# Optimization experiments

Hardware: AMD Instinct MI355X
Metric: run time of the kernel (lower is better)

Reference implementation:

```python
import jax, jax.numpy as jnp
import numpy as np

N_NODES = 50000
N_EDGES = 800000
HIDDEN = 128
IN_DIM = 128
OUT_DIM = 40
N_LAYERS = 3


def setup_inputs() -> dict:
    key = jax.random.key(0)
    ks = jax.random.split(key, 8)
    s = 1.0 / np.sqrt(HIDDEN)
    return {
        "x": jax.random.normal(ks[0], (N_NODES, IN_DIM), jnp.float32),
        "edge_index": jax.random.randint(ks[1], (2, N_EDGES), 0, N_NODES, jnp.int32),
        "W_in": jax.random.normal(ks[2], (IN_DIM, HIDDEN), jnp.float32) * s,
        "b_in": jnp.zeros((HIDDEN,), jnp.float32),
        "Wl": jax.random.normal(ks[3], (N_LAYERS, HIDDEN, HIDDEN), jnp.float32) * s,
        "Wr": jax.random.normal(ks[4], (N_LAYERS, HIDDEN, HIDDEN), jnp.float32) * s,
        "bl": jnp.zeros((N_LAYERS, HIDDEN), jnp.float32),
        "Wc1": jax.random.normal(ks[5], (HIDDEN, HIDDEN), jnp.float32) * s,
        "bc1": jnp.zeros((HIDDEN,), jnp.float32),
        "Wc2": jax.random.normal(ks[6], (HIDDEN, OUT_DIM), jnp.float32) * s,
        "bc2": jnp.zeros((OUT_DIM,), jnp.float32),
    }


def reference(x, edge_index, W_in, b_in, Wl, Wr, bl, Wc1, bc1, Wc2, bc2):
    src, dst = edge_index[0], edge_index[1]
    n = x.shape[0]
    # in-degree for mean aggregation (clamped to 1 for isolated nodes)
    deg = jax.ops.segment_sum(jnp.ones_like(src, x.dtype), dst, num_segments=n)
    deg_inv = (1.0 / jnp.maximum(deg, 1.0))[:, None]  # [N,1]

    h = x @ W_in + b_in  # lin1; dropout is identity in eval mode
    js = []
    for i in range(N_LAYERS):
        # GraphSAGE-mean: gather neighbor feats, scatter-mean, self + neighbor linear
        agg = jax.ops.segment_sum(h[src], dst, num_segments=n) * deg_inv
        h = jax.nn.relu(h @ Wl[i] + agg @ Wr[i] + bl[i])
        js.append(h)  # skip ops are identity; fix_last appends last layer directly

    x5 = js[0] + js[1] + js[2]  # layer aggregator 'l_sum' with linear activation
    hc = jax.nn.relu(x5 @ Wc1 + bc1)
    return hc @ Wc2 + bc2  # logits [N, OUT_DIM]
```

## Files before the change

### kernel.cpp

```cpp
#include <hip/hip_runtime.h>

#define NN   50000
#define NE   800000
#define HID  128
#define OUTD 40
#define NBLK 196
#define LIN_BLKS ((NN + 127) / 128)
#define DEG_BLKS ((NE + 255) / 256)

typedef float f32x4  __attribute__((ext_vector_type(4)));
typedef int   i32x4  __attribute__((ext_vector_type(4)));
typedef short bf16x8 __attribute__((ext_vector_type(8)));

__device__ __forceinline__ f32x4 mfma(bf16x8 a, bf16x8 b, f32x4 c) {
  return __builtin_amdgcn_mfma_f32_16x16x32_bf16(a, b, c, 0, 0, 0);
}
__device__ __forceinline__ unsigned short f2bf(float f) {
  unsigned u = __builtin_bit_cast(unsigned, f);
  u += 0x7fffu + ((u >> 16) & 1u);
  return (unsigned short)(u >> 16);
}
__device__ __forceinline__ unsigned pack2(float lo, float hi) {
  return (unsigned)f2bf(lo) | ((unsigned)f2bf(hi) << 16);
}
__device__ __forceinline__ float bflo(unsigned v){ return __builtin_bit_cast(float, v << 16); }
__device__ __forceinline__ float bfhi(unsigned v){ return __builtin_bit_cast(float, v & 0xffff0000u); }
__device__ __forceinline__ void acc8(float* a, uint4 v) {
  a[0] += bflo(v.x); a[1] += bfhi(v.x);
  a[2] += bflo(v.y); a[3] += bfhi(v.y);
  a[4] += bflo(v.z); a[5] += bfhi(v.z);
  a[6] += bflo(v.w); a[7] += bfhi(v.w);
}

__global__ void k_blocksum(const int* __restrict__ deg, int* __restrict__ bsum) {
  __shared__ int s[256];
  int t = threadIdx.x, i = blockIdx.x * 256 + t;
  s[t] = (i < NN) ? deg[i] : 0;
  __syncthreads();
  for (int o = 128; o > 0; o >>= 1) { if (t < o) s[t] += s[t + o]; __syncthreads(); }
  if (t == 0) bsum[blockIdx.x] = s[0];
}

__global__ void k_scan3(const int* __restrict__ deg, const int* __restrict__ bsum,
                        int* __restrict__ offs, float* __restrict__ dinv) {
  __shared__ int sb[256];
  __shared__ int s[256];
  int t = threadIdx.x, i = blockIdx.x * 256 + t;
  sb[t] = (t < NBLK && t < blockIdx.x) ? bsum[t] : 0;
  int v = (i < NN) ? deg[i] : 0;
  s[t] = v;
  __syncthreads();
  for (int o = 128; o > 0; o >>= 1) { if (t < o) sb[t] += sb[t + o]; __syncthreads(); }
  for (int o = 1; o < 256; o <<= 1) {
    int x = (t >= o) ? s[t - o] : 0;
    __syncthreads(); s[t] += x; __syncthreads();
  }
  int off = sb[0] + s[t] - v;
  if (i < NN) {
    offs[i] = off;
    dinv[i] = 1.0f / (float)(v > 0 ? v : 1);
  }
  if (i == 0) offs[NN] = NE;
}

__global__ void k_fill(const int* __restrict__ src, const int* __restrict__ dst,
                       const int* __restrict__ pos, const int* __restrict__ offs,
                       int* __restrict__ csr) {
  int i = blockIdx.x * blockDim.x + threadIdx.x;
  if (i < NE) {
    csr[offs[dst[i]] + pos[i]] = src[i];
  }
}

__global__ void k_prep(const float* __restrict__ Win, const float* __restrict__ Wl,
                       const float* __restrict__ Wr, const float* __restrict__ Wc1,
                       const float* __restrict__ Wc2, unsigned short* __restrict__ wt,
                       int* __restrict__ deg) {
  int idx = blockIdx.x * 256 + threadIdx.x;
  if (idx < NN) deg[idx] = 0;
  const int NMAIN = 8 * 16384;
  if (idx >= NMAIN + 48 * 128) return;
  float v;
  if (idx < NMAIN) {
    int m = idx >> 14, rem = idx & 16383;
    int n = rem >> 7, k = rem & 127;
    const float* s;
    if (m == 0) s = Win;
    else if (m <= 3) s = Wl + (m - 1) * 16384;
    else if (m <= 6) s = Wr + (m - 4) * 16384;
    else s = Wc1;
    v = s[k * 128 + n];
  } else {
    int rem = idx - NMAIN;
    int n = rem >> 7, k = rem & 127;
    v = (n < OUTD) ? Wc2[k * OUTD + n] : 0.f;
  }
  wt[idx] = f2bf(v);
}

__device__ __forceinline__ void lin_in_body(int bid, const float* __restrict__ x,
                                            const unsigned short* __restrict__ Wt,
                                            const float* __restrict__ bias,
                                            unsigned short* __restrict__ hout) {
  const int lane = threadIdx.x & 63, w = threadIdx.x >> 6;
  const int wr = w >> 1, wc = w & 1;
  const int r15 = lane & 15, khi = lane >> 4;
  const int mbase = bid * 128 + wr * 64, nbase = wc * 64;
  f32x4 acc[4][4] = {};
#pragma unroll
  for (int ks = 0; ks < 4; ++ks) {
    const int kk = ks * 32 + khi * 8;
    bf16x8 af[4], bq[4];
#pragma unroll
    for (int i = 0; i < 4; i++) {
      int row = mbase + i * 16 + r15; row = row < NN ? row : NN - 1;
      const f32x4* p = (const f32x4*)(x + row * HID + kk);
      f32x4 lo = p[0], hi = p[1];
      i32x4 t;
      t[0] = pack2(lo[0], lo[1]); t[1] = pack2(lo[2], lo[3]);
      t[2] = pack2(hi[0], hi[1]); t[3] = pack2(hi[2], hi[3]);
      af[i] = __builtin_bit_cast(bf16x8, t);
    }
#pragma unroll
    for (int j = 0; j < 4; j++) {
      int col = nbase + j * 16 + r15;
      bq[j] = *(const bf16x8*)(Wt + col * HID + kk);
    }
#pragma unroll
    for (int i = 0; i < 4; i++)
#pragma unroll
      for (int j = 0; j < 4; j++) acc[i][j] = mfma(af[i], bq[j], acc[i][j]);
  }
  float b4[4];
#pragma unroll
  for (int j = 0; j < 4; j++) b4[j] = bias[nbase + j * 16 + r15];
#pragma unroll
  for (int i = 0; i < 4; i++) {
    const int rb = mbase + i * 16 + khi * 4;
#pragma unroll
    for (int e = 0; e < 4; e++) {
      const int r = rb + e;
      if (r < NN) {
#pragma unroll
        for (int j = 0; j < 4; j++)
          hout[r * HID + nbase + j * 16 + r15] = f2bf(acc[i][j][e] + b4[j]);
      }
    }
  }
}

__global__ __launch_bounds__(256) void k_deg_lin(const int* __restrict__ dst,
                                                 int* __restrict__ deg,
                                                 int* __restrict__ pos,
                                                 const float* __restrict__ x,
                                                 const unsigned short* __restrict__ Wt,
                                                 const float* __restrict__ bias,
                                                 unsigned short* __restrict__ hout) {
  if (blockIdx.x < LIN_BLKS) {
    lin_in_body(blockIdx.x, x, Wt, bias, hout);
  } else {
    int i = (blockIdx.x - LIN_BLKS) * 256 + threadIdx.x;
    if (i < NE) pos[i] = atomicAdd(&deg[dst[i]], 1);
  }
}

__global__ __launch_bounds__(256) void k_agg(const unsigned short* __restrict__ h,
                                             const int* __restrict__ csr,
                                             const int* __restrict__ offs,
                                             const float* __restrict__ dinv,
                                             unsigned short* __restrict__ agg) {
  const int lane = threadIdx.x & 63;
  const int c = lane & 15;
  const int q = lane >> 4;
  int gw = (blockIdx.x * 256 + (int)threadIdx.x) >> 6;
  const int nw = (gridDim.x * 256) >> 6;
  const uint4* h4 = (const uint4*)h;
  uint4* ag4 = (uint4*)agg;
  for (int n = gw; n < NN; n += nw) {
    const int s = offs[n], e = offs[n + 1];
    float a[8] = {0, 0, 0, 0, 0, 0, 0, 0};
    float b[8] = {0, 0, 0, 0, 0, 0, 0, 0};
    int k = s;
    int ia = 0, ib = 0;
    bool have = (k + 8 <= e);
    if (have) { ia = csr[k + q]; ib = csr[k + 4 + q]; }
    while (have) {
      uint4 va = h4[ia * 16 + c];
      uint4 vb = h4[ib * 16 + c];
      k += 8;
      have = (k + 8 <= e);
      if (have) { ia = csr[k + q]; ib = csr[k + 4 + q]; }
      acc8(a, va);
      acc8(b, vb);
    }
    for (; k < e; k += 4) {
      if (k + q < e) {
        uint4 v = h4[csr[k + q] * 16 + c];
        acc8(a, v);
      }
    }
    float f0 = a[0] + b[0], f1 = a[1] + b[1], f2 = a[2] + b[2], f3 = a[3] + b[3];
    float f4 = a[4] + b[4], f5 = a[5] + b[5], f6 = a[6] + b[6], f7 = a[7] + b[7];
    f0 += __shfl_xor(f0, 16); f1 += __shfl_xor(f1, 16);
    f2 += __shfl_xor(f2, 16); f3 += __shfl_xor(f3, 16);
    f4 += __shfl_xor(f4, 16); f5 += __shfl_xor(f5, 16);
    f6 += __shfl_xor(f6, 16); f7 += __shfl_xor(f7, 16);
    f0 += __shfl_xor(f0, 32); f1 += __shfl_xor(f1, 32);
    f2 += __shfl_xor(f2, 32); f3 += __shfl_xor(f3, 32);
    f4 += __shfl_xor(f4, 32); f5 += __shfl_xor(f5, 32);
    f6 += __shfl_xor(f6, 32); f7 += __shfl_xor(f7, 32);
    if (q == 0) {
      float di = dinv[n];
      uint4 o;
      o.x = pack2(f0 * di, f1 * di);
      o.y = pack2(f2 * di, f3 * di);
      o.z = pack2(f4 * di, f5 * di);
      o.w = pack2(f6 * di, f7 * di);
      ag4[n * 16 + c] = o;
    }
  }
}

__global__ __launch_bounds__(256) void k_layer(const unsigned short* __restrict__ hp,
                                               const unsigned short* __restrict__ ag,
                                               const unsigned short* __restrict__ WtL,
                                               const unsigned short* __restrict__ WtR,
                                               const float* __restrict__ bias,
                                               unsigned short* __restrict__ hout) {
  const int lane = threadIdx.x & 63, w = threadIdx.x >> 6;
  const int wr = w >> 1, wc = w & 1;
  const int r15 = lane & 15, khi = lane >> 4;
  const int mbase = blockIdx.x * 128 + wr * 64, nbase = wc * 64;
  f32x4 acc[4][4] = {};
#pragma unroll
  for (int ph = 0; ph < 2; ++ph) {
    const unsigned short* A = ph ? ag : hp;
    const unsigned short* B = ph ? WtR : WtL;
#pragma unroll
    for (int ks = 0; ks < 4; ++ks) {
      const int kk = ks * 32 + khi * 8;
      bf16x8 af[4], bq[4];
#pragma unroll
      for (int i = 0; i < 4; i++) {
        int row = mbase + i * 16 + r15; row = row < NN ? row : NN - 1;
        af[i] = *(const bf16x8*)(A + row * HID + kk);
      }
#pragma unroll
      for (int j = 0; j < 4; j++) {
        int col = nbase + j * 16 + r15;
        bq[j] = *(const bf16x8*)(B + col * HID + kk);
      }
#pragma unroll
      for (int i = 0; i < 4; i++)
#pragma unroll
        for (int j = 0; j < 4; j++) acc[i][j] = mfma(af[i], bq[j], acc[i][j]);
    }
  }
  float b4[4];
#pragma unroll
  for (int j = 0; j < 4; j++) b4[j] = bias[nbase + j * 16 + r15];
#pragma unroll
  for (int i = 0; i < 4; i++) {
    const int rb = mbase + i * 16 + khi * 4;
#pragma unroll
    for (int e = 0; e < 4; e++) {
      const int r = rb + e;
      if (r < NN) {
#pragma unroll
        for (int j = 0; j < 4; j++) {
          float v = acc[i][j][e] + b4[j];
          v = fmaxf(v, 0.f);
          hout[r * HID + nbase + j * 16 + r15] = f2bf(v);
        }
      }
    }
  }
}

__global__ __launch_bounds__(256) void k_cls(const unsigned short* __restrict__ h1,
                                             const unsigned short* __restrict__ h2,
                                             const unsigned short* __restrict__ h3,
                                             const unsigned short* __restrict__ WtC1,
                                             const float* __restrict__ bc1,
                                             const unsigned short* __restrict__ WtC2,
                                             const float* __restrict__ bc2,
                                             float* __restrict__ out) {
  __shared__ unsigned short hc[128 * 136];
  const int lane = threadIdx.x & 63, w = threadIdx.x >> 6;
  const int wr = w >> 1, wc = w & 1;
  const int r15 = lane & 15, khi = lane >> 4;
  const int mbase = blockIdx.x * 128 + wr * 64, nbase = wc * 64;
  {
    f32x4 acc[4][4] = {};
#pragma unroll
    for (int ks = 0; ks < 4; ++ks) {
      const int kk = ks * 32 + khi * 8;
      bf16x8 af[4], bq[4];
#pragma unroll
      for (int i = 0; i < 4; i++) {
        int row = mbase + i * 16 + r15; row = row < NN ? row : NN - 1;
        i32x4 u = *(const i32x4*)(h1 + row * HID + kk);
        i32x4 v = *(const i32x4*)(h2 + row * HID + kk);
        i32x4 q = *(const i32x4*)(h3 + row * HID + kk);
        i32x4 t;
#pragma unroll
        for (int cc = 0; cc < 4; cc++) {
          unsigned uu = u[cc], vv = v[cc], qq = q[cc];
          t[cc] = pack2(bflo(uu) + bflo(vv) + bflo(qq), bfhi(uu) + bfhi(vv) + bfhi(qq));
        }
        af[i] = __builtin_bit_cast(bf16x8, t);
      }
#pragma unroll
      for (int j = 0; j < 4; j++) {
        int col = nbase + j * 16 + r15;
        bq[j] = *(const bf16x8*)(WtC1 + col * HID + kk);
      }
#pragma unroll
      for (int i = 0; i < 4; i++)
#pragma unroll
        for (int j = 0; j < 4; j++) acc[i][j] = mfma(af[i], bq[j], acc[i][j]);
    }
    float b4[4];
#pragma unroll
    for (int j = 0; j < 4; j++) b4[j] = bc1[nbase + j * 16 + r15];
#pragma unroll
    for (int i = 0; i < 4; i++) {
      const int rT = wr * 64 + i * 16 + khi * 4;
#pragma unroll
      for (int e = 0; e < 4; e++) {
#pragma unroll
        for (int j = 0; j < 4; j++) {
          float v = fmaxf(acc[i][j][e] + b4[j], 0.f);
          hc[(rT + e) * 136 + nbase + j * 16 + r15] = f2bf(v);
        }
      }
    }
  }
  __syncthreads();
  {
    f32x4 a2[2][3] = {};
#pragma unroll
    for (int ks = 0; ks < 4; ++ks) {
      const int kk = ks * 32 + khi * 8;
      bf16x8 af[2], bq[3];
#pragma unroll
      for (int i = 0; i < 2; i++) {
        int rT = w * 32 + i * 16 + r15;
        af[i] = *(const bf16x8*)&hc[rT * 136 + kk];
      }
#pragma unroll
      for (int j = 0; j < 3; j++) {
        int col = j * 16 + r15;
        bq[j] = *(const bf16x8*)(WtC2 + col * HID + kk);
      }
#pragma unroll
      for (int i = 0; i < 2; i++)
#pragma unroll
        for (int j = 0; j < 3; j++) a2[i][j] = mfma(af[i], bq[j], a2[i][j]);
    }
#pragma unroll
    for (int j = 0; j < 3; j++) {
      const int col = j * 16 + r15;
      const float b = (col < OUTD) ? bc2[col] : 0.f;
#pragma unroll
      for (int i = 0; i < 2; i++) {
        const int rT = w * 32 + i * 16 + khi * 4;
#pragma unroll
        for (int e = 0; e < 4; e++) {
          const int gr = blockIdx.x * 128 + rT + e;
          if (gr < NN && col < OUTD) out[gr * OUTD + col] = a2[i][j][e] + b;
        }
      }
    }
  }
}

extern "C" void kernel_launch(void* const* d_in, const int* in_sizes, int n_in,
                              void* d_out, int out_size, void* d_ws, size_t ws_size,
                              hipStream_t stream) {
  (void)in_sizes; (void)n_in; (void)out_size; (void)ws_size;
  const float* x   = (const float*)d_in[0];
  const int*   ei  = (const int*)d_in[1];
  const float* Win = (const float*)d_in[2];
  const float* bin = (const float*)d_in[3];
  const float* Wl  = (const float*)d_in[4];
  const float* Wr  = (const float*)d_in[5];
  const float* bl  = (const float*)d_in[6];
  const float* Wc1 = (const float*)d_in[7];
  const float* bc1 = (const float*)d_in[8];
  const float* Wc2 = (const float*)d_in[9];
  const float* bc2 = (const float*)d_in[10];
  float* out = (float*)d_out;

  char* ws = (char*)d_ws;
  size_t off = 0;
  auto take = [&](size_t bytes) -> char* {
    char* p = ws + off; off = (off + bytes + 255) & ~(size_t)255; return p;
  };
  int* deg        = (int*)take((size_t)NN * 4);
  int* offs       = (int*)take((size_t)(NN + 1) * 4);
  int* pos        = (int*)take((size_t)NE * 4);
  int* bsum       = (int*)take(256 * 4);
  float* dinv     = (float*)take((size_t)NN * 4);
  int* csr        = (int*)take((size_t)NE * 4);
  unsigned short* wt  = (unsigned short*)take((size_t)(8 * 16384 + 48 * 128) * 2);
  unsigned short* h0  = (unsigned short*)take((size_t)NN * HID * 2);
  unsigned short* h1  = (unsigned short*)take((size_t)NN * HID * 2);
  unsigned short* h2  = (unsigned short*)take((size_t)NN * HID * 2);
  unsigned short* h3  = (unsigned short*)take((size_t)NN * HID * 2);
  unsigned short* agg = (unsigned short*)take((size_t)NN * HID * 2);

  const int* esrc = ei;
  const int* edst = ei + NE;

  k_prep<<<(8 * 16384 + 48 * 128 + 255) / 256, 256, 0, stream>>>(Win, Wl, Wr, Wc1, Wc2, wt, deg);
  k_deg_lin<<<LIN_BLKS + DEG_BLKS, 256, 0, stream>>>(edst, deg, pos, x, wt, bin, h0);
  k_blocksum<<<NBLK, 256, 0, stream>>>(deg, bsum);
  k_scan3<<<NBLK, 256, 0, stream>>>(deg, bsum, offs, dinv);
  k_fill<<<(NE + 255) / 256, 256, 0, stream>>>(esrc, edst, pos, offs, csr);

  unsigned short* hs[4] = {h0, h1, h2, h3};
  for (int i = 0; i < 3; i++) {
    k_agg<<<2048, 256, 0, stream>>>(hs[i], csr, offs, dinv, agg);
    k_layer<<<(NN + 127) / 128, 256, 0, stream>>>(hs[i], agg, wt + (1 + i) * 16384,
                                                  wt + (4 + i) * 16384, bl + i * HID, hs[i + 1]);
  }
  k_cls<<<(NN + 127) / 128, 256, 0, stream>>>(h1, h2, h3, wt + 7 * 16384, bc1,
                                              wt + 8 * 16384, bc2, out);
}
```

Baseline: 234.6 us.

## Gather neighbor features from FP8 copies in the aggregation kernel

```diff
diff --git a/kernel.cpp b/kernel.cpp
--- a/kernel.cpp
+++ b/kernel.cpp
@@ -1,4 +1,5 @@
 #include <hip/hip_runtime.h>
+#include <hip/hip_fp8.h>
 
 #define NN   50000
 #define NE   800000
@@ -25,11 +26,20 @@
 }
 __device__ __forceinline__ float bflo(unsigned v){ return __builtin_bit_cast(float, v << 16); }
 __device__ __forceinline__ float bfhi(unsigned v){ return __builtin_bit_cast(float, v & 0xffff0000u); }
-__device__ __forceinline__ void acc8(float* a, uint4 v) {
-  a[0] += bflo(v.x); a[1] += bfhi(v.x);
-  a[2] += bflo(v.y); a[3] += bfhi(v.y);
-  a[4] += bflo(v.z); a[5] += bfhi(v.z);
-  a[6] += bflo(v.w); a[7] += bfhi(v.w);
+__device__ __forceinline__ unsigned char f2fp8(float f) {
+  return (unsigned char)__hip_fp8_e4m3(f).__x;
+}
+__device__ __forceinline__ void accfp8(float* a, uint4 v) {
+  unsigned u[4] = {v.x, v.y, v.z, v.w};
+#pragma unroll
+  for (int i = 0; i < 4; i++) {
+#pragma unroll
+    for (int b = 0; b < 4; b++) {
+      __hip_fp8_e4m3 t;
+      t.__x = (__hip_fp8_storage_t)((u[i] >> (8 * b)) & 0xffu);
+      a[i * 4 + b] += (float)t;
+    }
+  }
 }
 
 __global__ void k_blocksum(const int* __restrict__ deg, int* __restrict__ bsum) {
@@ -101,7 +111,8 @@
 __device__ __forceinline__ void lin_in_body(int bid, const float* __restrict__ x,
                                             const unsigned short* __restrict__ Wt,
                                             const float* __restrict__ bias,
-                                            unsigned short* __restrict__ hout) {
+                                            unsigned short* __restrict__ hout,
+                                            unsigned char* __restrict__ h8out) {
   const int lane = threadIdx.x & 63, w = threadIdx.x >> 6;
   const int wr = w >> 1, wc = w & 1;
   const int r15 = lane & 15, khi = lane >> 4;
@@ -142,8 +153,12 @@
       const int r = rb + e;
       if (r < NN) {
 #pragma unroll
-        for (int j = 0; j < 4; j++)
-          hout[r * HID + nbase + j * 16 + r15] = f2bf(acc[i][j][e] + b4[j]);
+        for (int j = 0; j < 4; j++) {
+          float v = acc[i][j][e] + b4[j];
+          const int col = nbase + j * 16 + r15;
+          hout[r * HID + col] = f2bf(v);
+          h8out[r * HID + col] = f2fp8(v);
+        }
       }
     }
   }
@@ -155,68 +170,71 @@
                                                  const float* __restrict__ x,
                                                  const unsigned short* __restrict__ Wt,
                                                  const float* __restrict__ bias,
-                                                 unsigned short* __restrict__ hout) {
+                                                 unsigned short* __restrict__ hout,
+                                                 unsigned char* __restrict__ h8out) {
   if (blockIdx.x < LIN_BLKS) {
-    lin_in_body(blockIdx.x, x, Wt, bias, hout);
+    lin_in_body(blockIdx.x, x, Wt, bias, hout, h8out);
   } else {
     int i = (blockIdx.x - LIN_BLKS) * 256 + threadIdx.x;
     if (i < NE) pos[i] = atomicAdd(&deg[dst[i]], 1);
   }
 }
 
-__global__ __launch_bounds__(256) void k_agg(const unsigned short* __restrict__ h,
+__global__ __launch_bounds__(256) void k_agg(const unsigned char* __restrict__ h8,
                                              const int* __restrict__ csr,
                                              const int* __restrict__ offs,
                                              const float* __restrict__ dinv,
                                              unsigned short* __restrict__ agg) {
   const int lane = threadIdx.x & 63;
-  const int c = lane & 15;
-  const int q = lane >> 4;
+  const int c8 = lane & 7;
+  const int o8 = lane >> 3;
   int gw = (blockIdx.x * 256 + (int)threadIdx.x) >> 6;
   const int nw = (gridDim.x * 256) >> 6;
-  const uint4* h4 = (const uint4*)h;
+  const uint4* h4 = (const uint4*)h8;
   uint4* ag4 = (uint4*)agg;
   for (int n = gw; n < NN; n += nw) {
     const int s = offs[n], e = offs[n + 1];
-    float a[8] = {0, 0, 0, 0, 0, 0, 0, 0};
-    float b[8] = {0, 0, 0, 0, 0, 0, 0, 0};
+    float a[16];
+#pragma unroll
+    for (int j = 0; j < 16; j++) a[j] = 0.f;
     int k = s;
     int ia = 0, ib = 0;
-    bool have = (k + 8 <= e);
-    if (have) { ia = csr[k + q]; ib = csr[k + 4 + q]; }
+    bool have = (k + 16 <= e);
+    if (have) { ia = csr[k + o8]; ib = csr[k + 8 + o8]; }
     while (have) {
-      uint4 va = h4[ia * 16 + c];
-      uint4 vb = h4[ib * 16 + c];
-      k += 8;
-      have = (k + 8 <= e);
-      if (have) { ia = csr[k + q]; ib = csr[k + 4 + q]; }
-      acc8(a, va);
-      acc8(b, vb);
-    }
-    for (; k < e; k += 4) {
-      if (k + q < e) {
-        uint4 v = h4[csr[k + q] * 16 + c];
-        acc8(a, v);
-      }
-    }
-    float f0 = a[0] + b[0], f1 = a[1] + b[1], f2 = a[2] + b[2], f3 = a[3] + b[3];
-    float f4 = a[4] + b[4], f5 = a[5] + b[5], f6 = a[6] + b[6], f7 = a[7] + b[7];
-    f0 += __shfl_xor(f0, 16); f1 += __shfl_xor(f1, 16);
-    f2 += __shfl_xor(f2, 16); f3 += __shfl_xor(f3, 16);
-    f4 += __shfl_xor(f4, 16); f5 += __shfl_xor(f5, 16);
-    f6 += __shfl_xor(f6, 16); f7 += __shfl_xor(f7, 16);
-    f0 += __shfl_xor(f0, 32); f1 += __shfl_xor(f1, 32);
-    f2 += __shfl_xor(f2, 32); f3 += __shfl_xor(f3, 32);
-    f4 += __shfl_xor(f4, 32); f5 += __shfl_xor(f5, 32);
-    f6 += __shfl_xor(f6, 32); f7 += __shfl_xor(f7, 32);
-    if (q == 0) {
+      uint4 va = h4[ia * 8 + c8];
+      uint4 vb = h4[ib * 8 + c8];
+      k += 16;
+      have = (k + 16 <= e);
+      if (have) { ia = csr[k + o8]; ib = csr[k + 8 + o8]; }
+      accfp8(a, va);
+      accfp8(a, vb);
+    }
+    for (; k < e; k += 8) {
+      if (k + o8 < e) {
+        uint4 v = h4[csr[k + o8] * 8 + c8];
+        accfp8(a, v);
+      }
+    }
+#pragma unroll
+    for (int j = 0; j < 16; j++) {
+      a[j] += __shfl_xor(a[j], 8);
+      a[j] += __shfl_xor(a[j], 16);
+      a[j] += __shfl_xor(a[j], 32);
+    }
+    if (o8 == 0) {
       float di = dinv[n];
-      uint4 o;
-      o.x = pack2(f0 * di, f1 * di);
-      o.y = pack2(f2 * di, f3 * di);
-      o.z = pack2(f4 * di, f5 * di);
-      o.w = pack2(f6 * di, f7 * di);
-      ag4[n * 16 + c] = o;
+      uint4 o0, o1;
+      o0.x = pack2(a[0] * di, a[1] * di);
+      o0.y = pack2(a[2] * di, a[3] * di);
+      o0.z = pack2(a[4] * di, a[5] * di);
+      o0.w = pack2(a[6] * di, a[7] * di);
+      o1.x = pack2(a[8] * di, a[9] * di);
+      o1.y = pack2(a[10] * di, a[11] * di);
+      o1.z = pack2(a[12] * di, a[13] * di);
+      o1.w = pack2(a[14] * di, a[15] * di);
+      ag4[n * 16 + c8 * 2 + 0] = o0;
+      ag4[n * 16 + c8 * 2 + 1] = o1;
     }
   }
 }
@@ -226,7 +244,8 @@
                                                const unsigned short* __restrict__ WtL,
                                                const unsigned short* __restrict__ WtR,
                                                const float* __restrict__ bias,
-                                               unsigned short* __restrict__ hout) {
+                                               unsigned short* __restrict__ hout,
+                                               unsigned char* __restrict__ h8out) {
   const int lane = threadIdx.x & 63, w = threadIdx.x >> 6;
   const int wr = w >> 1, wc = w & 1;
   const int r15 = lane & 15, khi = lane >> 4;
@@ -270,7 +289,9 @@
         for (int j = 0; j < 4; j++) {
           float v = acc[i][j][e] + b4[j];
           v = fmaxf(v, 0.f);
-          hout[r * HID + nbase + j * 16 + r15] = f2bf(v);
+          const int col = nbase + j * 16 + r15;
+          hout[r * HID + col] = f2bf(v);
+          h8out[r * HID + col] = f2fp8(v);
         }
       }
     }
@@ -409,21 +430,27 @@
   unsigned short* h2  = (unsigned short*)take((size_t)NN * HID * 2);
   unsigned short* h3  = (unsigned short*)take((size_t)NN * HID * 2);
   unsigned short* agg = (unsigned short*)take((size_t)NN * HID * 2);
+  unsigned char* h8_0 = (unsigned char*)take((size_t)NN * HID);
+  unsigned char* h8_1 = (unsigned char*)take((size_t)NN * HID);
+  unsigned char* h8_2 = (unsigned char*)take((size_t)NN * HID);
 
   const int* esrc = ei;
   const int* edst = ei + NE;
 
   k_prep<<<(8 * 16384 + 48 * 128 + 255) / 256, 256, 0, stream>>>(Win, Wl, Wr, Wc1, Wc2, wt, deg);
-  k_deg_lin<<<LIN_BLKS + DEG_BLKS, 256, 0, stream>>>(edst, deg, pos, x, wt, bin, h0);
+  k_deg_lin<<<LIN_BLKS + DEG_BLKS, 256, 0, stream>>>(edst, deg, pos, x, wt, bin, h0, h8_0);
   k_blocksum<<<NBLK, 256, 0, stream>>>(deg, bsum);
   k_scan3<<<NBLK, 256, 0, stream>>>(deg, bsum, offs, dinv);
   k_fill<<<(NE + 255) / 256, 256, 0, stream>>>(esrc, edst, pos, offs, csr);
 
   unsigned short* hs[4] = {h0, h1, h2, h3};
+  unsigned char* h8s[3] = {h8_0, h8_1, h8_2};
   for (int i = 0; i < 3; i++) {
-    k_agg<<<2048, 256, 0, stream>>>(hs[i], csr, offs, dinv, agg);
+    k_agg<<<2048, 256, 0, stream>>>(h8s[i], csr, offs, dinv, agg);
+    unsigned char* h8next = (i < 2) ? h8s[i + 1] : h8_0;
     k_layer<<<(NN + 127) / 128, 256, 0, stream>>>(hs[i], agg, wt + (1 + i) * 16384,
-                                                  wt + (4 + i) * 16384, bl + i * HID, hs[i + 1]);
+                                                  wt + (4 + i) * 16384, bl + i * HID,
+                                                  hs[i + 1], h8next);
   }
   k_cls<<<(NN + 127) / 128, 256, 0, stream>>>(h1, h2, h3, wt + 7 * 16384, bc1,
                                               wt + 8 * 16384, bc2, out);
```

New measurement: 276.1 us. 1.18x slower.

## Overlap self-linear GEMM with neighbor aggregation in one launch

Applied to the files above, without the earlier changes.

```diff
diff --git a/kernel.cpp b/kernel.cpp
--- a/kernel.cpp
+++ b/kernel.cpp
@@ -7,6 +7,7 @@
 #define NBLK 196
 #define LIN_BLKS ((NN + 127) / 128)
 #define DEG_BLKS ((NE + 255) / 256)
+#define AGG_BLKS 2048
 
 typedef float f32x4  __attribute__((ext_vector_type(4)));
 typedef int   i32x4  __attribute__((ext_vector_type(4)));
@@ -25,6 +26,7 @@
 }
 __device__ __forceinline__ float bflo(unsigned v){ return __builtin_bit_cast(float, v << 16); }
 __device__ __forceinline__ float bfhi(unsigned v){ return __builtin_bit_cast(float, v & 0xffff0000u); }
+__device__ __forceinline__ float bf2f(unsigned short u){ return __builtin_bit_cast(float, (unsigned)u << 16); }
 __device__ __forceinline__ void acc8(float* a, uint4 v) {
   a[0] += bflo(v.x); a[1] += bfhi(v.x);
   a[2] += bflo(v.y); a[3] += bfhi(v.y);
@@ -164,16 +166,16 @@
   }
 }
 
-__global__ __launch_bounds__(256) void k_agg(const unsigned short* __restrict__ h,
-                                             const int* __restrict__ csr,
-                                             const int* __restrict__ offs,
-                                             const float* __restrict__ dinv,
-                                             unsigned short* __restrict__ agg) {
+__device__ __forceinline__ void agg_body(int abid, const unsigned short* __restrict__ h,
+                                         const int* __restrict__ csr,
+                                         const int* __restrict__ offs,
+                                         const float* __restrict__ dinv,
+                                         unsigned short* __restrict__ agg) {
   const int lane = threadIdx.x & 63;
   const int c = lane & 15;
   const int q = lane >> 4;
-  int gw = (blockIdx.x * 256 + (int)threadIdx.x) >> 6;
-  const int nw = (gridDim.x * 256) >> 6;
+  int gw = (abid * 256 + (int)threadIdx.x) >> 6;
+  const int nw = (AGG_BLKS * 256) >> 6;
   const uint4* h4 = (const uint4*)h;
   uint4* ag4 = (uint4*)agg;
   for (int n = gw; n < NN; n += nw) {
@@ -221,40 +223,41 @@
   }
 }
 
-__global__ __launch_bounds__(256) void k_layer(const unsigned short* __restrict__ hp,
-                                               const unsigned short* __restrict__ ag,
-                                               const unsigned short* __restrict__ WtL,
-                                               const unsigned short* __restrict__ WtR,
-                                               const float* __restrict__ bias,
-                                               unsigned short* __restrict__ hout) {
+__global__ __launch_bounds__(256) void k_agg_lin(const unsigned short* __restrict__ h,
+                                                 const int* __restrict__ csr,
+                                                 const int* __restrict__ offs,
+                                                 const float* __restrict__ dinv,
+                                                 unsigned short* __restrict__ agg,
+                                                 const unsigned short* __restrict__ WtL,
+                                                 const float* __restrict__ bias,
+                                                 unsigned short* __restrict__ part) {
+  if (blockIdx.x >= LIN_BLKS) {
+    agg_body(blockIdx.x - LIN_BLKS, h, csr, offs, dinv, agg);
+    return;
+  }
   const int lane = threadIdx.x & 63, w = threadIdx.x >> 6;
   const int wr = w >> 1, wc = w & 1;
   const int r15 = lane & 15, khi = lane >> 4;
   const int mbase = blockIdx.x * 128 + wr * 64, nbase = wc * 64;
   f32x4 acc[4][4] = {};
 #pragma unroll
-  for (int ph = 0; ph < 2; ++ph) {
-    const unsigned short* A = ph ? ag : hp;
-    const unsigned short* B = ph ? WtR : WtL;
-#pragma unroll
-    for (int ks = 0; ks < 4; ++ks) {
-      const int kk = ks * 32 + khi * 8;
-      bf16x8 af[4], bq[4];
-#pragma unroll
-      for (int i = 0; i < 4; i++) {
-        int row = mbase + i * 16 + r15; row = row < NN ? row : NN - 1;
-        af[i] = *(const bf16x8*)(A + row * HID + kk);
-      }
-#pragma unroll
-      for (int j = 0; j < 4; j++) {
-        int col = nbase + j * 16 + r15;
-        bq[j] = *(const bf16x8*)(B + col * HID + kk);
-      }
-#pragma unroll
-      for (int i = 0; i < 4; i++)
-#pragma unroll
-        for (int j = 0; j < 4; j++) acc[i][j] = mfma(af[i], bq[j], acc[i][j]);
-    }
+  for (int ks = 0; ks < 4; ++ks) {
+    const int kk = ks * 32 + khi * 8;
+    bf16x8 af[4], bq[4];
+#pragma unroll
+    for (int i = 0; i < 4; i++) {
+      int row = mbase + i * 16 + r15; row = row < NN ? row : NN - 1;
+      af[i] = *(const bf16x8*)(h + row * HID + kk);
+    }
+#pragma unroll
+    for (int j = 0; j < 4; j++) {
+      int col = nbase + j * 16 + r15;
+      bq[j] = *(const bf16x8*)(WtL + col * HID + kk);
+    }
+#pragma unroll
+    for (int i = 0; i < 4; i++)
+#pragma unroll
+      for (int j = 0; j < 4; j++) acc[i][j] = mfma(af[i], bq[j], acc[i][j]);
   }
   float b4[4];
 #pragma unroll
@@ -267,10 +270,54 @@
       const int r = rb + e;
       if (r < NN) {
 #pragma unroll
+        for (int j = 0; j < 4; j++)
+          part[r * HID + nbase + j * 16 + r15] = f2bf(acc[i][j][e] + b4[j]);
+      }
+    }
+  }
+}
+
+__global__ __launch_bounds__(256) void k_layer2(const unsigned short* __restrict__ part,
+                                                const unsigned short* __restrict__ ag,
+                                                const unsigned short* __restrict__ WtR,
+                                                unsigned short* __restrict__ hout) {
+  const int lane = threadIdx.x & 63, w = threadIdx.x >> 6;
+  const int wr = w >> 1, wc = w & 1;
+  const int r15 = lane & 15, khi = lane >> 4;
+  const int mbase = blockIdx.x * 128 + wr * 64, nbase = wc * 64;
+  f32x4 acc[4][4] = {};
+#pragma unroll
+  for (int ks = 0; ks < 4; ++ks) {
+    const int kk = ks * 32 + khi * 8;
+    bf16x8 af[4], bq[4];
+#pragma unroll
+    for (int i = 0; i < 4; i++) {
+      int row = mbase + i * 16 + r15; row = row < NN ? row : NN - 1;
+      af[i] = *(const bf16x8*)(ag + row * HID + kk);
+    }
+#pragma unroll
+    for (int j = 0; j < 4; j++) {
+      int col = nbase + j * 16 + r15;
+      bq[j] = *(const bf16x8*)(WtR + col * HID + kk);
+    }
+#pragma unroll
+    for (int i = 0; i < 4; i++)
+#pragma unroll
+      for (int j = 0; j < 4; j++) acc[i][j] = mfma(af[i], bq[j], acc[i][j]);
+  }
+#pragma unroll
+  for (int i = 0; i < 4; i++) {
+    const int rb = mbase + i * 16 + khi * 4;
+#pragma unroll
+    for (int e = 0; e < 4; e++) {
+      const int r = rb + e;
+      if (r < NN) {
+#pragma unroll
         for (int j = 0; j < 4; j++) {
-          float v = acc[i][j][e] + b4[j];
+          const int col = nbase + j * 16 + r15;
+          float v = acc[i][j][e] + bf2f(part[r * HID + col]);
           v = fmaxf(v, 0.f);
-          hout[r * HID + nbase + j * 16 + r15] = f2bf(v);
+          hout[r * HID + col] = f2bf(v);
         }
       }
     }
@@ -409,6 +456,7 @@
   unsigned short* h2  = (unsigned short*)take((size_t)NN * HID * 2);
   unsigned short* h3  = (unsigned short*)take((size_t)NN * HID * 2);
   unsigned short* agg = (unsigned short*)take((size_t)NN * HID * 2);
+  unsigned short* part = (unsigned short*)take((size_t)NN * HID * 2);
 
   const int* esrc = ei;
   const int* edst = ei + NE;
@@ -421,9 +469,9 @@
 
   unsigned short* hs[4] = {h0, h1, h2, h3};
   for (int i = 0; i < 3; i++) {
-    k_agg<<<2048, 256, 0, stream>>>(hs[i], csr, offs, dinv, agg);
-    k_layer<<<(NN + 127) / 128, 256, 0, stream>>>(hs[i], agg, wt + (1 + i) * 16384,
-                                                  wt + (4 + i) * 16384, bl + i * HID, hs[i + 1]);
+    k_agg_lin<<<LIN_BLKS + AGG_BLKS, 256, 0, stream>>>(hs[i], csr, offs, dinv, agg,
+                                                       wt + (1 + i) * 16384, bl + i * HID, part);
+    k_layer2<<<LIN_BLKS, 256, 0, stream>>>(part, agg, wt + (4 + i) * 16384, hs[i + 1]);
   }
   k_cls<<<(NN + 127) / 128, 256, 0, stream>>>(h1, h2, h3, wt + 7 * 16384, bc1,
                                               wt + 8 * 16384, bc2, out);
```

After: 326.8 us. 1.39x slower.
